# Optimization experiments

Hardware: AMD Instinct MI355X
Metric: run time of the kernel (lower is better)

The kernel has to match this reference:

```python
import jax, jax.numpy as jnp
import numpy as np

BLOCK_SIZE = 256
N_EMBD = 384
HEAD_SIZE = 384
B = 256
T = 256


def setup_inputs() -> dict:
    key = jax.random.key(0)
    kx, kk, kq, kv = jax.random.split(key, 4)
    scale = 1.0 / np.sqrt(N_EMBD)
    x = jax.random.normal(kx, (B, T, N_EMBD), dtype=jnp.float32)
    Wk = jax.random.normal(kk, (HEAD_SIZE, N_EMBD), dtype=jnp.float32) * scale
    Wq = jax.random.normal(kq, (HEAD_SIZE, N_EMBD), dtype=jnp.float32) * scale
    Wv = jax.random.normal(kv, (HEAD_SIZE, N_EMBD), dtype=jnp.float32) * scale
    return {"x": x, "Wk": Wk, "Wq": Wq, "Wv": Wv}


def reference(x, Wk, Wq, Wv):
    # Single-head causal self-attention; equals forward_with_cache at prefill
    # (fresh cache, cache_index=0, T tokens) and forward_no_cache.
    # Linear layers are bias-free: y = x @ W.T
    k = jnp.einsum('btc,hc->bth', x, Wk)  # [B,T,H]
    q = jnp.einsum('btc,hc->bth', x, Wq)
    v = jnp.einsum('btc,hc->bth', x, Wv)
    inv_sqrt_hs = jnp.asarray(HEAD_SIZE, x.dtype) ** -0.5
    wei = jnp.einsum('bth,bsh->bts', q, k) * inv_sqrt_hs  # [B,T,T]
    causal = jnp.tril(jnp.ones((T, T), dtype=bool))
    wei = jnp.where(causal, wei, jnp.asarray(-jnp.inf, wei.dtype))
    wei = jax.nn.softmax(wei, axis=-1)
    # dropout is identity in eval mode
    out = jnp.einsum('bts,bsh->bth', wei, v)  # [B,T,H]
    return out
```

## Files before the change

### kernel.cpp

```cpp
#include <hip/hip_runtime.h>

#define B_ 256
#define T_ 256
#define C_ 384
#define H_ 384

typedef float f4 __attribute__((ext_vector_type(4)));
typedef float f32x4 __attribute__((ext_vector_type(4)));
typedef short bf8 __attribute__((ext_vector_type(8)));
typedef short s8v __attribute__((ext_vector_type(8)));
typedef short s4v __attribute__((ext_vector_type(4)));

__device__ __forceinline__ short f2bf(float f) {
  unsigned u = __builtin_bit_cast(unsigned, f);
  u += 0x7FFFu + ((u >> 16) & 1u);
  return (short)(u >> 16);
}

__device__ __forceinline__ void gload_lds16(const void* g, void* l) {
  __builtin_amdgcn_global_load_lds(
      (const __attribute__((address_space(1))) unsigned int*)g,
      (__attribute__((address_space(3))) unsigned int*)l, 16, 0, 0);
}

__global__ __launch_bounds__(256) void convert_kernel(
    const float* __restrict__ x, const float* __restrict__ wk,
    const float* __restrict__ wq, const float* __restrict__ wv,
    short* __restrict__ xb, short* __restrict__ wb) {
  const int NXG = (B_ * T_ * C_) / 8;
  const int NWG = (H_ * C_) / 8;
  const int total = NXG + 3 * NWG;
  for (int g = blockIdx.x * 256 + threadIdx.x; g < total; g += gridDim.x * 256) {
    const float* src;
    short* dst;
    if (g < NXG) {
      src = x + (size_t)g * 8;
      dst = xb + (size_t)g * 8;
    } else {
      int h = g - NXG;
      int wsel = h / NWG;
      int o = h - wsel * NWG;
      const float* wp = wsel == 0 ? wk : (wsel == 1 ? wq : wv);
      src = wp + (size_t)o * 8;
      dst = wb + (size_t)wsel * (H_ * C_) + (size_t)o * 8;
    }
    f4 f0 = *(const f4*)src;
    f4 f1 = *(const f4*)(src + 4);
    s8v r;
    r[0] = f2bf(f0[0]); r[1] = f2bf(f0[1]); r[2] = f2bf(f0[2]); r[3] = f2bf(f0[3]);
    r[4] = f2bf(f1[0]); r[5] = f2bf(f1[1]); r[6] = f2bf(f1[2]); r[7] = f2bf(f1[3]);
    *(s8v*)dst = r;
  }
}

__global__ __launch_bounds__(256) void proj_gemm(
    const short* __restrict__ xb, const short* __restrict__ wb,
    short* __restrict__ kb, short* __restrict__ qbuf, short* __restrict__ vt) {
  __shared__ __align__(16) short lA[128 * 64];
  __shared__ __align__(16) short lB[128 * 64];
  const int tid = threadIdx.x;
  const int cpx = 4608 / 8;
  const int bid = blockIdx.x;
  const int swz = (bid & 7) * cpx + (bid >> 3);
  const int nb = swz % 9;
  const int mb = swz / 9;
  const int m0 = mb * 128, gn0 = nb * 128;
  const int w = tid >> 6, l = tid & 63;
  const int wr = w >> 1, wc = w & 1;
  f32x4 acc[4][4] = {};
  for (int kc = 0; kc < 6; ++kc) {
    const int k0 = kc * 64;
#pragma unroll
    for (int j = 0; j < 4; ++j) {
      const int flat = j * 256 + tid;
      const int row = flat >> 3;
      const int colg = ((flat & 7) ^ (row & 7)) * 8;
      gload_lds16(xb + (size_t)(m0 + row) * C_ + k0 + colg, (char*)lA + flat * 16);
      gload_lds16(wb + (size_t)(gn0 + row) * C_ + k0 + colg, (char*)lB + flat * 16);
    }
    __syncthreads();
#pragma unroll
    for (int ks = 0; ks < 2; ++ks) {
      const int kg = ks * 4 + (l >> 4);
      bf8 av[4], bv[4];
#pragma unroll
      for (int mt = 0; mt < 4; ++mt) {
        const int ra = wr * 64 + mt * 16 + (l & 15);
        av[mt] = *(const bf8*)&lA[ra * 64 + ((kg ^ (ra & 7)) << 3)];
      }
#pragma unroll
      for (int nt = 0; nt < 4; ++nt) {
        const int rb = wc * 64 + nt * 16 + (l & 15);
        bv[nt] = *(const bf8*)&lB[rb * 64 + ((kg ^ (rb & 7)) << 3)];
      }
#pragma unroll
      for (int mt = 0; mt < 4; ++mt)
#pragma unroll
        for (int nt = 0; nt < 4; ++nt)
          acc[mt][nt] = __builtin_amdgcn_mfma_f32_16x16x32_bf16(
              av[mt], bv[nt], acc[mt][nt], 0, 0, 0);
    }
    __syncthreads();
  }
  const int proj = nb / 3;
  const int gcb = (nb % 3) * 128 + wc * 64 + (l & 15);
  const int tok0 = m0 + wr * 64 + ((l >> 4) * 4);
  if (proj < 2) {
    short* dst = proj == 0 ? kb : qbuf;
#pragma unroll
    for (int mt = 0; mt < 4; ++mt)
#pragma unroll
      for (int nt = 0; nt < 4; ++nt)
#pragma unroll
        for (int r = 0; r < 4; ++r)
          dst[(size_t)(tok0 + mt * 16 + r) * H_ + gcb + nt * 16] =
              f2bf(acc[mt][nt][r]);
  } else {
    const int bb = tok0 >> 8;
    const int tl0 = tok0 & 255;
#pragma unroll
    for (int mt = 0; mt < 4; ++mt)
#pragma unroll
      for (int nt = 0; nt < 4; ++nt) {
        s4v pk;
        pk[0] = f2bf(acc[mt][nt][0]); pk[1] = f2bf(acc[mt][nt][1]);
        pk[2] = f2bf(acc[mt][nt][2]); pk[3] = f2bf(acc[mt][nt][3]);
        *(s4v*)&vt[(size_t)bb * (H_ * T_) + (size_t)(gcb + nt * 16) * T_ +
                   tl0 + mt * 16] = pk;
      }
  }
}

__global__ __launch_bounds__(256) void attn_kernel(
    const short* __restrict__ qbuf, const short* __restrict__ kb,
    const short* __restrict__ vt, float* __restrict__ out) {
  __shared__ __align__(16) char smem[40960];
  short* Kl = (short*)smem;
  short* Ql = (short*)(smem + 32768);
  short* Pl = (short*)smem;
  const int b = blockIdx.x >> 2;
  const int qi = blockIdx.x & 3;
  const int t0 = qi * 64;
  const int SKV = t0 + 64;
  const int ntile = SKV >> 4;
  const int tid = threadIdx.x;
  const int w = tid >> 6, l = tid & 63;
  f32x4 sa[16] = {};
  for (int hc = 0; hc < 6; ++hc) {
    const int h0 = hc * 64;
#pragma unroll
    for (int j = 0; j < 2; ++j) {
      const int flat = j * 256 + tid;
      const int row = flat >> 3;
      const int colg = ((flat & 7) ^ (row & 7)) * 8;
      gload_lds16(qbuf + (size_t)(b * T_ + t0 + row) * H_ + h0 + colg,
                  (char*)Ql + flat * 16);
    }
    const int kiss = SKV >> 5;
    for (int j = 0; j < kiss; ++j) {
      const int flat = j * 256 + tid;
      const int row = flat >> 3;
      const int colg = ((flat & 7) ^ (row & 7)) * 8;
      gload_lds16(kb + (size_t)(b * T_ + row) * H_ + h0 + colg,
                  (char*)Kl + flat * 16);
    }
    __syncthreads();
#pragma unroll
    for (int ks = 0; ks < 2; ++ks) {
      const int kg = ks * 4 + (l >> 4);
      const int rq = w * 16 + (l & 15);
      bf8 av = *(const bf8*)&Ql[rq * 64 + ((kg ^ (rq & 7)) << 3)];
#pragma unroll
      for (int nt = 0; nt < 16; ++nt)
        if (nt < ntile) {
          const int rk = nt * 16 + (l & 15);
          bf8 bv = *(const bf8*)&Kl[rk * 64 + ((kg ^ (rk & 7)) << 3)];
          sa[nt] = __builtin_amdgcn_mfma_f32_16x16x32_bf16(av, bv, sa[nt], 0, 0, 0);
        }
    }
    __syncthreads();
  }
  const float scale = 0.05103103630798287f;
  const int rbl = w * 16 + (l >> 4) * 4;
#pragma unroll
  for (int r = 0; r < 4; ++r) {
    const int prow = rbl + r;
    const int trow = t0 + prow;
    float vv[16];
    float m = -3.0e38f;
#pragma unroll
    for (int nt = 0; nt < 16; ++nt)
      if (nt < ntile) {
        const int col = nt * 16 + (l & 15);
        float v = sa[nt][r] * scale;
        if (col > trow) v = -3.0e38f;
        vv[nt] = v;
        m = fmaxf(m, v);
      }
    m = fmaxf(m, __shfl_xor(m, 1));
    m = fmaxf(m, __shfl_xor(m, 2));
    m = fmaxf(m, __shfl_xor(m, 4));
    m = fmaxf(m, __shfl_xor(m, 8));
    float s = 0.f;
#pragma unroll
    for (int nt = 0; nt < 16; ++nt)
      if (nt < ntile) {
        vv[nt] = __expf(vv[nt] - m);
        s += vv[nt];
      }
    s += __shfl_xor(s, 1);
    s += __shfl_xor(s, 2);
    s += __shfl_xor(s, 4);
    s += __shfl_xor(s, 8);
    const float inv = 1.0f / s;
    const int sw = (prow & 7) << 3;
#pragma unroll
    for (int nt = 0; nt < 16; ++nt)
      if (nt < ntile) {
        const int col = nt * 16 + (l & 15);
        Pl[prow * 256 + (col ^ sw)] = f2bf(vv[nt] * inv);
      }
  }
  __syncthreads();
  f32x4 o[4][6] = {};
  const int nks = SKV >> 5;
  for (int ks = 0; ks < nks; ++ks) {
    const int kk = ks * 32 + (l >> 4) * 8;
    bf8 av[4];
#pragma unroll
    for (int mt = 0; mt < 4; ++mt) {
      const int rp = mt * 16 + (l & 15);
      av[mt] = *(const bf8*)&Pl[rp * 256 + (kk ^ ((rp & 7) << 3))];
    }
#pragma unroll
    for (int nt = 0; nt < 6; ++nt) {
      const int d = w * 96 + nt * 16 + (l & 15);
      bf8 bv = *(const bf8*)&vt[(size_t)b * (H_ * T_) + (size_t)d * T_ + kk];
#pragma unroll
      for (int mt = 0; mt < 4; ++mt)
        o[mt][nt] = __builtin_amdgcn_mfma_f32_16x16x32_bf16(av[mt], bv, o[mt][nt], 0, 0, 0);
    }
  }
#pragma unroll
  for (int mt = 0; mt < 4; ++mt) {
    const int tok = b * T_ + t0 + mt * 16 + (l >> 4) * 4;
#pragma unroll
    for (int nt = 0; nt < 6; ++nt) {
      const int d = w * 96 + nt * 16 + (l & 15);
#pragma unroll
      for (int r = 0; r < 4; ++r)
        out[(size_t)(tok + r) * H_ + d] = o[mt][nt][r];
    }
  }
}

extern "C" void kernel_launch(void* const* d_in, const int* in_sizes, int n_in,
                              void* d_out, int out_size, void* d_ws, size_t ws_size,
                              hipStream_t stream) {
  (void)in_sizes; (void)n_in; (void)out_size; (void)ws_size;
  const float* x = (const float*)d_in[0];
  const float* wk = (const float*)d_in[1];
  const float* wq = (const float*)d_in[2];
  const float* wv = (const float*)d_in[3];
  float* out = (float*)d_out;
  char* ws = (char*)d_ws;
  const size_t SZ = (size_t)B_ * T_ * H_ * 2;
  short* kbuf = (short*)ws;
  short* qbuf = (short*)(ws + SZ);
  short* vt   = (short*)(ws + 2 * SZ);
  short* xb = (short*)d_out;
  short* wb = (short*)((char*)d_out + SZ);
  convert_kernel<<<2048, 256, 0, stream>>>(x, wk, wq, wv, xb, wb);
  proj_gemm<<<4608, 256, 0, stream>>>(xb, wb, kbuf, qbuf, vt);
  attn_kernel<<<1024, 256, 0, stream>>>(qbuf, kbuf, vt, out);
}
```

Baseline: 339.6 us.

## Triple-buffer projection GEMM with 256x128 tiles and swizzle attention blocks

The projection GEMM moves to 512-thread blocks with 256-row A tiles and a 3-stage LDS ring. Async global-to-LDS loads are issued ahead and gated by explicit vmcnt waits, so loads overlap MFMA work. MFMA bursts are wrapped in setprio, and attention block indices are remapped through an XCD-style swizzle. The larger LDS footprint (about 144KB) may limit blocks per CU, and the hand-written vmcnt counts must match the per-stage load count.

```diff
diff --git a/kernel.cpp b/kernel.cpp
--- a/kernel.cpp
+++ b/kernel.cpp
@@ -53,54 +53,85 @@
   }
 }
 
-__global__ __launch_bounds__(256) void proj_gemm(
+__global__ __launch_bounds__(512) void proj_gemm(
     const short* __restrict__ xb, const short* __restrict__ wb,
     short* __restrict__ kb, short* __restrict__ qbuf, short* __restrict__ vt) {
-  __shared__ __align__(16) short lA[128 * 64];
-  __shared__ __align__(16) short lB[128 * 64];
+  __shared__ __align__(16) short lA[3][256 * 64];
+  __shared__ __align__(16) short lB[3][128 * 64];
   const int tid = threadIdx.x;
-  const int cpx = 4608 / 8;
   const int bid = blockIdx.x;
-  const int swz = (bid & 7) * cpx + (bid >> 3);
+  const int swz = (bid & 7) * 288 + (bid >> 3);
   const int nb = swz % 9;
   const int mb = swz / 9;
-  const int m0 = mb * 128, gn0 = nb * 128;
+  const int m0 = mb * 256, gn0 = nb * 128;
   const int w = tid >> 6, l = tid & 63;
   const int wr = w >> 1, wc = w & 1;
-  f32x4 acc[4][4] = {};
-  for (int kc = 0; kc < 6; ++kc) {
-    const int k0 = kc * 64;
+
+  auto STAGE = [&](int buf, int t) {
+    const int k0 = t * 64;
 #pragma unroll
     for (int j = 0; j < 4; ++j) {
-      const int flat = j * 256 + tid;
+      const int flat = j * 512 + tid;
       const int row = flat >> 3;
       const int colg = ((flat & 7) ^ (row & 7)) * 8;
-      gload_lds16(xb + (size_t)(m0 + row) * C_ + k0 + colg, (char*)lA + flat * 16);
-      gload_lds16(wb + (size_t)(gn0 + row) * C_ + k0 + colg, (char*)lB + flat * 16);
-    }
-    __syncthreads();
-#pragma unroll
-    for (int ks = 0; ks < 2; ++ks) {
-      const int kg = ks * 4 + (l >> 4);
-      bf8 av[4], bv[4];
-#pragma unroll
-      for (int mt = 0; mt < 4; ++mt) {
-        const int ra = wr * 64 + mt * 16 + (l & 15);
-        av[mt] = *(const bf8*)&lA[ra * 64 + ((kg ^ (ra & 7)) << 3)];
-      }
-#pragma unroll
-      for (int nt = 0; nt < 4; ++nt) {
-        const int rb = wc * 64 + nt * 16 + (l & 15);
-        bv[nt] = *(const bf8*)&lB[rb * 64 + ((kg ^ (rb & 7)) << 3)];
-      }
-#pragma unroll
-      for (int mt = 0; mt < 4; ++mt)
-#pragma unroll
-        for (int nt = 0; nt < 4; ++nt)
-          acc[mt][nt] = __builtin_amdgcn_mfma_f32_16x16x32_bf16(
-              av[mt], bv[nt], acc[mt][nt], 0, 0, 0);
-    }
-    __syncthreads();
+      gload_lds16(xb + (size_t)(m0 + row) * C_ + k0 + colg,
+                  (char*)&lA[buf][0] + flat * 16);
+    }
+#pragma unroll
+    for (int j = 0; j < 2; ++j) {
+      const int flat = j * 512 + tid;
+      const int row = flat >> 3;
+      const int colg = ((flat & 7) ^ (row & 7)) * 8;
+      gload_lds16(wb + (size_t)(gn0 + row) * C_ + k0 + colg,
+                  (char*)&lB[buf][0] + flat * 16);
+    }
+  };
+
+  f32x4 acc[4][4] = {};
+  STAGE(0, 0);
+  STAGE(1, 1);
+  STAGE(2, 2);
+#pragma unroll
+  for (int t = 0; t < 6; ++t) {
+    const int cur = t % 3;
+    if (t < 4)      asm volatile("s_waitcnt vmcnt(12)" ::: "memory");
+    else if (t == 4) asm volatile("s_waitcnt vmcnt(6)" ::: "memory");
+    else             asm volatile("s_waitcnt vmcnt(0)" ::: "memory");
+    __builtin_amdgcn_s_barrier();
+    __builtin_amdgcn_sched_barrier(0);
+    const short* A = &lA[cur][0];
+    const short* Bt = &lB[cur][0];
+#pragma unroll
+    for (int q = 0; q < 4; ++q) {
+      const int mtp = q >> 1, ntp = q & 1;
+      bf8 av[2][2], bv[2][2];
+#pragma unroll
+      for (int ks = 0; ks < 2; ++ks) {
+        const int kg = ks * 4 + (l >> 4);
+#pragma unroll
+        for (int i = 0; i < 2; ++i) {
+          const int ra = wr * 64 + (mtp * 2 + i) * 16 + (l & 15);
+          av[ks][i] = *(const bf8*)&A[ra * 64 + ((kg ^ (ra & 7)) << 3)];
+          const int rb = wc * 64 + (ntp * 2 + i) * 16 + (l & 15);
+          bv[ks][i] = *(const bf8*)&Bt[rb * 64 + ((kg ^ (rb & 7)) << 3)];
+        }
+      }
+      __builtin_amdgcn_s_setprio(1);
+#pragma unroll
+      for (int ks = 0; ks < 2; ++ks)
+#pragma unroll
+        for (int i = 0; i < 2; ++i)
+#pragma unroll
+          for (int jj = 0; jj < 2; ++jj)
+            acc[mtp * 2 + i][ntp * 2 + jj] =
+                __builtin_amdgcn_mfma_f32_16x16x32_bf16(
+                    av[ks][i], bv[ks][jj], acc[mtp * 2 + i][ntp * 2 + jj],
+                    0, 0, 0);
+      __builtin_amdgcn_s_setprio(0);
+    }
+    __builtin_amdgcn_sched_barrier(0);
+    __builtin_amdgcn_s_barrier();
+    if (t < 3) STAGE(cur, t + 3);
   }
   const int proj = nb / 3;
   const int gcb = (nb % 3) * 128 + wc * 64 + (l & 15);
@@ -138,8 +169,10 @@
   short* Kl = (short*)smem;
   short* Ql = (short*)(smem + 32768);
   short* Pl = (short*)smem;
-  const int b = blockIdx.x >> 2;
-  const int qi = blockIdx.x & 3;
+  const int bid = blockIdx.x;
+  const int swzb = (bid & 7) * 128 + (bid >> 3);
+  const int b = swzb >> 2;
+  const int qi = swzb & 3;
   const int t0 = qi * 64;
   const int SKV = t0 + 64;
   const int ntile = SKV >> 4;
@@ -271,6 +304,6 @@
   short* xb = (short*)d_out;
   short* wb = (short*)((char*)d_out + SZ);
   convert_kernel<<<2048, 256, 0, stream>>>(x, wk, wq, wv, xb, wb);
-  proj_gemm<<<4608, 256, 0, stream>>>(xb, wb, kbuf, qbuf, vt);
+  proj_gemm<<<2304, 512, 0, stream>>>(xb, wb, kbuf, qbuf, vt);
   attn_kernel<<<1024, 256, 0, stream>>>(qbuf, kbuf, vt, out);
 }
```

New measurement: 323.0 us. 1.05x faster.
